# Kernel optimization log

Measured on AMD Instinct MI355X. Metric: run time of the kernel, lower is better.

Reference implementation:

```python
import jax, jax.numpy as jnp
import numpy as np

N_NODES = 100000

def setup_inputs() -> dict:
    key = jax.random.key(0)
    k1, k2, k3, k4 = jax.random.split(key, 4)
    features = jax.random.normal(k1, (N_NODES, 128), dtype=jnp.float32)
    # Xavier-uniform init like the torch module
    limit = float(np.sqrt(6.0 / (128 + 64)))
    weight = jax.random.uniform(k2, (128, 64), dtype=jnp.float32, minval=-limit, maxval=limit)
    edge_index = jax.random.randint(k3, (2, 1600000), 0, N_NODES, dtype=jnp.int64)
    edge_weight = jax.random.uniform(k4, (1600000,), dtype=jnp.float32)
    return {"features": features, "weight": weight, "edge_index": edge_index, "edge_weight": edge_weight}

def reference(features, weight, edge_index, edge_weight):
    # support = X @ W  -> [N, out]
    support = features @ weight
    dst, src = edge_index[0], edge_index[1]
    # spmm(adj, support): out[i] = sum_j adj[i, j] * support[j]
    msgs = support[src] * edge_weight[:, None]            # [E, out]
    out = jax.ops.segment_sum(msgs, dst, num_segments=N_NODES)
    return jax.nn.relu(out)
```

## Files before the change

### kernel.cpp

```cpp
#include <hip/hip_runtime.h>
#include <hip/hip_bf16.h>

#define F_IN 128
#define F_OUT 64
#define NPB 128
#define LG_NPB 7
#define MAXB 1024
#define BIN_BLOCKS 784
#define BIN_THREADS 512
#define SORT_CAP 4096

typedef float  f32x4  __attribute__((ext_vector_type(4)));
typedef short  bf16x8 __attribute__((ext_vector_type(8)));

__device__ __forceinline__ short f2bf(float f) {
    union { __hip_bfloat16 h; short s; } u;
    u.h = __float2bfloat16(f);
    return u.s;
}

__global__ void __launch_bounds__(256) gnn_gemm_kernel(
    const float* __restrict__ X, const float* __restrict__ W,
    __hip_bfloat16* __restrict__ support, int n_rows) {
    const int lane   = threadIdx.x & 63;
    const int gwave  = (blockIdx.x * 256 + threadIdx.x) >> 6;
    const int nwaves = (gridDim.x * 256) >> 6;

    const int bcol = lane & 15;
    const int bk0  = (lane >> 4) * 8;
    bf16x8 bfrag[4][4];
#pragma unroll
    for (int ks = 0; ks < 4; ++ks)
#pragma unroll
        for (int ct = 0; ct < 4; ++ct) {
            bf16x8 f;
#pragma unroll
            for (int j = 0; j < 8; ++j)
                f[j] = f2bf(W[(ks * 32 + bk0 + j) * F_OUT + ct * 16 + bcol]);
            bfrag[ks][ct] = f;
        }

    const int arow = lane & 15;
    const int ak0  = (lane >> 4) * 8;
    const int crow = (lane >> 4) * 4;
    const int nmb  = n_rows >> 4;

    for (int mb = gwave; mb < nmb; mb += nwaves) {
        const int m0 = mb << 4;
        const float* xrow = X + (size_t)(m0 + arow) * F_IN + ak0;

        float4 xv[4][2];
#pragma unroll
        for (int ks = 0; ks < 4; ++ks) {
            xv[ks][0] = *reinterpret_cast<const float4*>(xrow + ks * 32);
            xv[ks][1] = *reinterpret_cast<const float4*>(xrow + ks * 32 + 4);
        }

        f32x4 acc[4];
#pragma unroll
        for (int ct = 0; ct < 4; ++ct) acc[ct] = (f32x4){0.f, 0.f, 0.f, 0.f};

#pragma unroll
        for (int ks = 0; ks < 4; ++ks) {
            bf16x8 af;
            af[0] = f2bf(xv[ks][0].x); af[1] = f2bf(xv[ks][0].y);
            af[2] = f2bf(xv[ks][0].z); af[3] = f2bf(xv[ks][0].w);
            af[4] = f2bf(xv[ks][1].x); af[5] = f2bf(xv[ks][1].y);
            af[6] = f2bf(xv[ks][1].z); af[7] = f2bf(xv[ks][1].w);
#pragma unroll
            for (int ct = 0; ct < 4; ++ct)
                acc[ct] = __builtin_amdgcn_mfma_f32_16x16x32_bf16(
                    af, bfrag[ks][ct], acc[ct], 0, 0, 0);
        }

#pragma unroll
        for (int ct = 0; ct < 4; ++ct)
#pragma unroll
            for (int r = 0; r < 4; ++r)
                support[(size_t)(m0 + crow + r) * F_OUT + ct * 16 + bcol] =
                    __float2bfloat16(acc[ct][r]);
    }
}

__global__ void __launch_bounds__(BIN_THREADS) gnn_bhist_kernel(
    const int* __restrict__ dst, int* __restrict__ gcounts, int n_edges, int n_buckets) {
    __shared__ int lcnt[MAXB];
    const int t = threadIdx.x;
    for (int i = t; i < MAXB; i += BIN_THREADS) lcnt[i] = 0;
    __syncthreads();
    int chunk = (n_edges + gridDim.x - 1) / gridDim.x;
    chunk = (chunk + 3) & ~3;
    const int c0 = min((int)(blockIdx.x * chunk), n_edges);
    const int c1 = min(c0 + chunk, n_edges);
    const int nv = (c1 - c0) >> 2;
    const int4* d4 = reinterpret_cast<const int4*>(dst + c0);
    for (int i = t; i < nv; i += BIN_THREADS) {
        const int4 d = d4[i];
        atomicAdd(&lcnt[d.x >> LG_NPB], 1);
        atomicAdd(&lcnt[d.y >> LG_NPB], 1);
        atomicAdd(&lcnt[d.z >> LG_NPB], 1);
        atomicAdd(&lcnt[d.w >> LG_NPB], 1);
    }
    for (int i = c0 + (nv << 2) + t; i < c1; i += BIN_THREADS)
        atomicAdd(&lcnt[dst[i] >> LG_NPB], 1);
    __syncthreads();
    for (int b = t; b < n_buckets; b += BIN_THREADS)
        if (lcnt[b]) atomicAdd(&gcounts[b], lcnt[b]);
}

__global__ void __launch_bounds__(1024) gnn_bscan_kernel(
    const int* __restrict__ gcounts, int* __restrict__ starts,
    int* __restrict__ cursor, int n_buckets) {
    __shared__ int s[1024];
    const int t = threadIdx.x;
    const int v = (t < n_buckets) ? gcounts[t] : 0;
    s[t] = v;
    __syncthreads();
    for (int off = 1; off < 1024; off <<= 1) {
        int x = (t >= off) ? s[t - off] : 0;
        __syncthreads();
        s[t] += x;
        __syncthreads();
    }
    if (t < n_buckets) {
        const int st = s[t] - v;
        starts[t] = st;
        cursor[t] = st;
    }
}

__global__ void __launch_bounds__(BIN_THREADS) gnn_place_kernel(
    const int* __restrict__ ei, const float* __restrict__ ew,
    int* __restrict__ cursor, int2* __restrict__ elistA, int n_edges, int n_buckets) {
    __shared__ int lcnt[MAXB];
    const int t = threadIdx.x;
    for (int i = t; i < MAXB; i += BIN_THREADS) lcnt[i] = 0;
    __syncthreads();
    int chunk = (n_edges + gridDim.x - 1) / gridDim.x;
    chunk = (chunk + 3) & ~3;
    const int c0 = min((int)(blockIdx.x * chunk), n_edges);
    const int c1 = min(c0 + chunk, n_edges);
    const int nv = (c1 - c0) >> 2;
    const int4* d4 = reinterpret_cast<const int4*>(ei + c0);

    for (int i = t; i < nv; i += BIN_THREADS) {
        const int4 d = d4[i];
        atomicAdd(&lcnt[d.x >> LG_NPB], 1);
        atomicAdd(&lcnt[d.y >> LG_NPB], 1);
        atomicAdd(&lcnt[d.z >> LG_NPB], 1);
        atomicAdd(&lcnt[d.w >> LG_NPB], 1);
    }
    for (int i = c0 + (nv << 2) + t; i < c1; i += BIN_THREADS)
        atomicAdd(&lcnt[ei[i] >> LG_NPB], 1);
    __syncthreads();
    for (int b = t; b < n_buckets; b += BIN_THREADS) {
        const int c = lcnt[b];
        if (c) lcnt[b] = atomicAdd(&cursor[b], c);
    }
    __syncthreads();

    const int4*   s4 = reinterpret_cast<const int4*>(ei + n_edges + c0);
    const float4* w4 = reinterpret_cast<const float4*>(ew + c0);
    for (int i = t; i < nv; i += BIN_THREADS) {
        const int4 d = d4[i];
        const int4 s = s4[i];
        const float4 w = w4[i];
        const int dd[4] = {d.x, d.y, d.z, d.w};
        const int ss[4] = {s.x, s.y, s.z, s.w};
        const float ww[4] = {w.x, w.y, w.z, w.w};
#pragma unroll
        for (int u = 0; u < 4; ++u) {
            const int b = dd[u] >> LG_NPB;
            const int pos = atomicAdd(&lcnt[b], 1);
            elistA[pos] = make_int2((ss[u] << LG_NPB) | (dd[u] & (NPB - 1)),
                                    __float_as_int(ww[u]));
        }
    }
    for (int i = c0 + (nv << 2) + t; i < c1; i += BIN_THREADS) {
        const int d = ei[i];
        const int s = ei[n_edges + i];
        const int b = d >> LG_NPB;
        const int pos = atomicAdd(&lcnt[b], 1);
        elistA[pos] = make_int2((s << LG_NPB) | (d & (NPB - 1)),
                                __float_as_int(ew[i]));
    }
}

__global__ void __launch_bounds__(512) gnn_sortpull_kernel(
    const __hip_bfloat16* __restrict__ support, const int2* __restrict__ elistA,
    const int* __restrict__ starts, const int* __restrict__ gcounts,
    float* __restrict__ out, int n_nodes) {
    __shared__ int2 smeta[SORT_CAP];
    __shared__ int hist[NPB];
    __shared__ int pfx[NPB];
    __shared__ int segs[NPB + 1];
    __shared__ int cur[NPB];
    const int t = threadIdx.x;
    const int b = blockIdx.x;
    const int bstart = starts[b];
    const int cnt    = min(gcounts[b], SORT_CAP);

    if (t < NPB) hist[t] = 0;
    __syncthreads();
    for (int i = t; i < cnt; i += 512)
        atomicAdd(&hist[elistA[bstart + i].x & (NPB - 1)], 1);
    __syncthreads();

    if (t < NPB) pfx[t] = hist[t];
    __syncthreads();
    for (int off = 1; off < NPB; off <<= 1) {
        int x = 0;
        if (t < NPB && t >= off) x = pfx[t - off];
        __syncthreads();
        if (t < NPB) pfx[t] += x;
        __syncthreads();
    }
    if (t < NPB) {
        const int st = pfx[t] - hist[t];
        segs[t] = st;
        cur[t]  = st;
    }
    if (t == 0) segs[NPB] = cnt;
    __syncthreads();

    for (int i = t; i < cnt; i += 512) {
        const int2 m = elistA[bstart + i];
        const int dlo = m.x & (NPB - 1);
        const int pos = atomicAdd(&cur[dlo], 1);
        smeta[pos] = make_int2(m.x & ~(NPB - 1), m.y);
    }
    __syncthreads();

    const char* sp = reinterpret_cast<const char*>(support);
    const int lane = t & 63;
    const int wave = t >> 6;
    for (int n = wave; n < NPB; n += 8) {
        const int node = b * NPB + n;
        if (node >= n_nodes) break;
        int e  = segs[n];
        const int e1 = segs[n + 1];
        float acc = 0.f;
        for (; e + 8 <= e1; e += 8) {
            int2 m[8];
#pragma unroll
            for (int u = 0; u < 8; ++u) m[u] = smeta[e + u];
            float g[8];
#pragma unroll
            for (int u = 0; u < 8; ++u)
                g[u] = __bfloat162float(
                    *reinterpret_cast<const __hip_bfloat16*>(sp + m[u].x + lane * 2));
#pragma unroll
            for (int u = 0; u < 8; ++u)
                acc = fmaf(__int_as_float(m[u].y), g[u], acc);
        }
        for (; e + 2 <= e1; e += 2) {
            const int2 m0 = smeta[e];
            const int2 m1 = smeta[e + 1];
            const float g0 = __bfloat162float(
                *reinterpret_cast<const __hip_bfloat16*>(sp + m0.x + lane * 2));
            const float g1 = __bfloat162float(
                *reinterpret_cast<const __hip_bfloat16*>(sp + m1.x + lane * 2));
            acc = fmaf(__int_as_float(m0.y), g0, acc);
            acc = fmaf(__int_as_float(m1.y), g1, acc);
        }
        if (e < e1) {
            const int2 m0 = smeta[e];
            acc = fmaf(__int_as_float(m0.y),
                       __bfloat162float(
                           *reinterpret_cast<const __hip_bfloat16*>(sp + m0.x + lane * 2)),
                       acc);
        }
        out[(size_t)node * F_OUT + lane] = fmaxf(acc, 0.f);
    }
}

extern "C" void kernel_launch(void* const* d_in, const int* in_sizes, int n_in,
                              void* d_out, int out_size, void* d_ws, size_t ws_size,
                              hipStream_t stream) {
    const float* X  = (const float*)d_in[0];
    const float* W  = (const float*)d_in[1];
    const int*   EI = (const int*)d_in[2];
    const float* EW = (const float*)d_in[3];
    float*       out = (float*)d_out;

    const int n_edges   = in_sizes[2] / 2;
    const int n_rows    = in_sizes[0] / F_IN;
    const int n_nodes   = out_size / F_OUT;
    const int n_buckets = (n_nodes + NPB - 1) >> LG_NPB;

    char* ws = (char*)d_ws;
    __hip_bfloat16* support = (__hip_bfloat16*)ws;
    size_t off = (size_t)n_rows * F_OUT * sizeof(__hip_bfloat16);
    int2* elistA = (int2*)(ws + off); off += (size_t)n_edges * sizeof(int2);
    int* gcounts = (int*)(ws + off);  off += MAXB * sizeof(int);
    int* starts  = (int*)(ws + off);  off += MAXB * sizeof(int);
    int* cursor  = (int*)(ws + off);

    hipMemsetAsync(gcounts, 0, (size_t)n_buckets * sizeof(int), stream);

    gnn_bhist_kernel<<<BIN_BLOCKS, BIN_THREADS, 0, stream>>>(EI, gcounts, n_edges, n_buckets);
    gnn_bscan_kernel<<<1, 1024, 0, stream>>>(gcounts, starts, cursor, n_buckets);
    gnn_place_kernel<<<BIN_BLOCKS, BIN_THREADS, 0, stream>>>(EI, EW, cursor, elistA, n_edges, n_buckets);
    gnn_gemm_kernel<<<512, 256, 0, stream>>>(X, W, support, n_rows);
    gnn_sortpull_kernel<<<n_buckets, 512, 0, stream>>>(support, elistA, starts, gcounts, out, n_nodes);
}
```

Before: 202.0 us.

## Stage bucketed edges in shared memory before coalesced scatter in place kernel

The place kernel now handles fixed chunks of 4000 edges per block. It sorts each chunk locally by bucket in shared memory, using a block-wide prefix scan plus a staging buffer, and then writes each bucket's run to its global slot contiguously. Before, every edge did a scattered 8-byte global write. The goal is to turn those random writes into mostly contiguous runs and cut write traffic inefficiency. In exchange the kernel uses much more shared memory (about 50KB), which lowers occupancy, and it adds an extra scan and several syncs.

Measured after the change: 197.6 us. -2.2%, faster.

```diff
diff --git a/kernel.cpp b/kernel.cpp
--- a/kernel.cpp
+++ b/kernel.cpp
@@ -9,6 +9,7 @@
 #define BIN_BLOCKS 784
 #define BIN_THREADS 512
 #define SORT_CAP 4096
+#define PLACE_CHUNK 4000
 
 typedef float  f32x4  __attribute__((ext_vector_type(4)));
 typedef short  bf16x8 __attribute__((ext_vector_type(8)));
@@ -129,39 +130,59 @@
     }
 }
 
-__global__ void __launch_bounds__(BIN_THREADS) gnn_place_kernel(
+__global__ void __launch_bounds__(512) gnn_place_kernel(
     const int* __restrict__ ei, const float* __restrict__ ew,
     int* __restrict__ cursor, int2* __restrict__ elistA, int n_edges, int n_buckets) {
-    __shared__ int lcnt[MAXB];
+    __shared__ int  lcnt[MAXB];
+    __shared__ int  ps[512];
+    __shared__ int  lstart[MAXB];
+    __shared__ int  cur[MAXB];
+    __shared__ int  gbase[MAXB];
+    __shared__ int2 stg[PLACE_CHUNK];
+    __shared__ unsigned short sbkt[PLACE_CHUNK];
     const int t = threadIdx.x;
-    for (int i = t; i < MAXB; i += BIN_THREADS) lcnt[i] = 0;
-    __syncthreads();
-    int chunk = (n_edges + gridDim.x - 1) / gridDim.x;
-    chunk = (chunk + 3) & ~3;
-    const int c0 = min((int)(blockIdx.x * chunk), n_edges);
-    const int c1 = min(c0 + chunk, n_edges);
-    const int nv = (c1 - c0) >> 2;
+    for (int i = t; i < MAXB; i += 512) lcnt[i] = 0;
+    __syncthreads();
+
+    const int c0  = min((int)(blockIdx.x * PLACE_CHUNK), n_edges);
+    const int c1  = min(c0 + PLACE_CHUNK, n_edges);
+    const int cnt = c1 - c0;
+    const int nv  = cnt >> 2;
     const int4* d4 = reinterpret_cast<const int4*>(ei + c0);
 
-    for (int i = t; i < nv; i += BIN_THREADS) {
+    for (int i = t; i < nv; i += 512) {
         const int4 d = d4[i];
         atomicAdd(&lcnt[d.x >> LG_NPB], 1);
         atomicAdd(&lcnt[d.y >> LG_NPB], 1);
         atomicAdd(&lcnt[d.z >> LG_NPB], 1);
         atomicAdd(&lcnt[d.w >> LG_NPB], 1);
     }
-    for (int i = c0 + (nv << 2) + t; i < c1; i += BIN_THREADS)
+    for (int i = c0 + (nv << 2) + t; i < c1; i += 512)
         atomicAdd(&lcnt[ei[i] >> LG_NPB], 1);
     __syncthreads();
-    for (int b = t; b < n_buckets; b += BIN_THREADS) {
-        const int c = lcnt[b];
-        if (c) lcnt[b] = atomicAdd(&cursor[b], c);
-    }
+
+    const int a0 = lcnt[2 * t];
+    const int a1 = lcnt[2 * t + 1];
+    ps[t] = a0 + a1;
+    __syncthreads();
+    for (int off = 1; off < 512; off <<= 1) {
+        int x = (t >= off) ? ps[t - off] : 0;
+        __syncthreads();
+        ps[t] += x;
+        __syncthreads();
+    }
+    const int pairbase = (t == 0) ? 0 : ps[t - 1];
+    lstart[2 * t]     = pairbase;
+    lstart[2 * t + 1] = pairbase + a0;
+    cur[2 * t]        = pairbase;
+    cur[2 * t + 1]    = pairbase + a0;
+    if (a0) gbase[2 * t]     = atomicAdd(&cursor[2 * t], a0);
+    if (a1) gbase[2 * t + 1] = atomicAdd(&cursor[2 * t + 1], a1);
     __syncthreads();
 
     const int4*   s4 = reinterpret_cast<const int4*>(ei + n_edges + c0);
     const float4* w4 = reinterpret_cast<const float4*>(ew + c0);
-    for (int i = t; i < nv; i += BIN_THREADS) {
+    for (int i = t; i < nv; i += 512) {
         const int4 d = d4[i];
         const int4 s = s4[i];
         const float4 w = w4[i];
@@ -171,18 +192,26 @@
 #pragma unroll
         for (int u = 0; u < 4; ++u) {
             const int b = dd[u] >> LG_NPB;
-            const int pos = atomicAdd(&lcnt[b], 1);
-            elistA[pos] = make_int2((ss[u] << LG_NPB) | (dd[u] & (NPB - 1)),
-                                    __float_as_int(ww[u]));
-        }
-    }
-    for (int i = c0 + (nv << 2) + t; i < c1; i += BIN_THREADS) {
+            const int pos = atomicAdd(&cur[b], 1);
+            stg[pos]  = make_int2((ss[u] << LG_NPB) | (dd[u] & (NPB - 1)),
+                                  __float_as_int(ww[u]));
+            sbkt[pos] = (unsigned short)b;
+        }
+    }
+    for (int i = c0 + (nv << 2) + t; i < c1; i += 512) {
         const int d = ei[i];
         const int s = ei[n_edges + i];
         const int b = d >> LG_NPB;
-        const int pos = atomicAdd(&lcnt[b], 1);
-        elistA[pos] = make_int2((s << LG_NPB) | (d & (NPB - 1)),
-                                __float_as_int(ew[i]));
+        const int pos = atomicAdd(&cur[b], 1);
+        stg[pos]  = make_int2((s << LG_NPB) | (d & (NPB - 1)),
+                              __float_as_int(ew[i]));
+        sbkt[pos] = (unsigned short)b;
+    }
+    __syncthreads();
+
+    for (int i = t; i < cnt; i += 512) {
+        const int b = sbkt[i];
+        elistA[gbase[b] + (i - lstart[b])] = stg[i];
     }
 }
 
@@ -298,9 +327,11 @@
 
     hipMemsetAsync(gcounts, 0, (size_t)n_buckets * sizeof(int), stream);
 
+    const int place_blocks = (n_edges + PLACE_CHUNK - 1) / PLACE_CHUNK;
+
     gnn_bhist_kernel<<<BIN_BLOCKS, BIN_THREADS, 0, stream>>>(EI, gcounts, n_edges, n_buckets);
     gnn_bscan_kernel<<<1, 1024, 0, stream>>>(gcounts, starts, cursor, n_buckets);
-    gnn_place_kernel<<<BIN_BLOCKS, BIN_THREADS, 0, stream>>>(EI, EW, cursor, elistA, n_edges, n_buckets);
+    gnn_place_kernel<<<place_blocks, 512, 0, stream>>>(EI, EW, cursor, elistA, n_edges, n_buckets);
     gnn_gemm_kernel<<<512, 256, 0, stream>>>(X, W, support, n_rows);
     gnn_sortpull_kernel<<<n_buckets, 512, 0, stream>>>(support, elistA, starts, gcounts, out, n_nodes);
 }
```
